# Optimization experiments

Hardware: AMD Instinct MI355X
Metric: run time of the kernel (lower is better)

## Reference

```python
import jax, jax.numpy as jnp
import numpy as np

N = 100000
E = 600000
IN_DIM = 128
HID = 128


def setup_inputs() -> dict:
    key = jax.random.key(0)
    ks = jax.random.split(key, 12)
    def lin(kw, fan_in, fan_out):
        # torch nn.Linear default init: U(-1/sqrt(fan_in), 1/sqrt(fan_in))
        bound = 1.0 / np.sqrt(fan_in)
        kw1, kw2 = jax.random.split(kw)
        w = jax.random.uniform(kw1, (fan_in, fan_out), jnp.float32, -bound, bound)
        b = jax.random.uniform(kw2, (fan_out,), jnp.float32, -bound, bound)
        return w, b
    x = jax.random.normal(ks[0], (N, IN_DIM), jnp.float32)
    edge_index = jax.random.randint(ks[1], (2, E), 0, N, jnp.int64)
    w1a, b1a = lin(ks[2], IN_DIM, HID)
    w1b, b1b = lin(ks[3], HID, HID)
    w2a, b2a = lin(ks[4], HID, HID)
    w2b, b2b = lin(ks[5], HID, HID)
    wo, bo = lin(ks[6], HID, 1)
    return {"x": x, "edge_index": edge_index,
            "w1a": w1a, "b1a": b1a, "w1b": w1b, "b1b": b1b,
            "w2a": w2a, "b2a": b2a, "w2b": w2b, "b2b": b2b,
            "wo": wo, "bo": bo}


def _gin_conv(x, src, dst, wa, ba, wb, bb):
    # sum-aggregate neighbor features: agg[dst] += x[src]; eps = 0 (GIN default)
    agg = jax.ops.segment_sum(x[src], dst, num_segments=N)
    h = x + agg
    h = jax.nn.relu(h @ wa + ba)
    return h @ wb + bb


def reference(x, edge_index, w1a, b1a, w1b, b1b, w2a, b2a, w2b, b2b, wo, bo):
    src, dst = edge_index[0], edge_index[1]
    h = _gin_conv(x, src, dst, w1a, b1a, w1b, b1b)
    h = _gin_conv(h, src, dst, w2a, b2a, w2b, b2b)
    return (h @ wo + bo).squeeze(-1)  # [N]
```

## Files before the change

### kernel.cpp

```cpp
#include <hip/hip_runtime.h>

typedef unsigned short u16;
typedef unsigned int u32;
typedef __bf16 bf16x8 __attribute__((ext_vector_type(8)));
typedef float f32x4 __attribute__((ext_vector_type(4)));

__device__ __forceinline__ u16 f2bf(float f) {
  union { float f; u32 u; } c; c.f = f;
  return (u16)((c.u + 0x7fffu + ((c.u >> 16) & 1u)) >> 16);
}
__device__ __forceinline__ float2 upk2(u32 v) {
  union { u32 u; float f; } a, b; a.u = v << 16; b.u = v & 0xffff0000u;
  return make_float2(a.f, b.f);
}
__device__ __forceinline__ u32 pk2(float x, float y) {
  return (u32)f2bf(x) | ((u32)f2bf(y) << 16);
}

__global__ __launch_bounds__(256) void k_prep(const float4* __restrict__ x4,
                                              uint2* __restrict__ xb,
                                              int n4,
                                              const int* __restrict__ dst,
                                              int* __restrict__ counts,
                                              int E, int histBlocks, int trBlocks,
                                              const float* __restrict__ w0,
                                              const float* __restrict__ w1,
                                              const float* __restrict__ w2,
                                              const float* __restrict__ w3,
                                              u16* __restrict__ wT) {
  int b = blockIdx.x, t = threadIdx.x;
  if ((b % 5) != 4) {
    int cb = b - b / 5;
    int i = cb * 256 + t;
    if (i < n4) {
      float4 v = x4[i];
      xb[i] = make_uint2(pk2(v.x, v.y), pk2(v.z, v.w));
    }
  } else {
    int k = b / 5;
    if (k < histBlocks) {
      int e = k * 256 + t;
      if (e < E) atomicAdd(&counts[dst[e]], 1);
    } else {
      int k2 = k - histBlocks;
      if (k2 < trBlocks) {
        int id = k2 * 256 + t;
        int w = id >> 14, rem = id & 16383;
        int nn = rem >> 7, kk = rem & 127;
        const float* s = (w == 0) ? w0 : (w == 1) ? w1 : (w == 2) ? w2 : w3;
        wT[id] = f2bf(s[kk * 128 + nn]);
      }
    }
  }
}

__global__ __launch_bounds__(256) void k_scan1(const int* __restrict__ counts,
                                               int* __restrict__ excl,
                                               int* __restrict__ partials, int n) {
  __shared__ int sh[256];
  int b = blockIdx.x, t = threadIdx.x;
  int base = b * 1024 + t * 4;
  int v[4];
#pragma unroll
  for (int j = 0; j < 4; ++j) { int i = base + j; v[j] = (i < n) ? counts[i] : 0; }
  int tot = v[0] + v[1] + v[2] + v[3];
  sh[t] = tot; __syncthreads();
  for (int off = 1; off < 256; off <<= 1) {
    int x = (t >= off) ? sh[t - off] : 0;
    __syncthreads();
    sh[t] += x;
    __syncthreads();
  }
  int run = sh[t] - tot;
#pragma unroll
  for (int j = 0; j < 4; ++j) {
    int i = base + j;
    if (i < n) excl[i] = run;
    run += v[j];
  }
  if (t == 255) partials[b] = sh[255];
}

__global__ __launch_bounds__(256) void k_scan23(int* __restrict__ rowstart,
                                                int* __restrict__ cursor,
                                                const int* __restrict__ partials,
                                                int n, int E, int nb) {
  __shared__ int sh[128];
  int t = threadIdx.x;
  int own = 0;
  if (t < 128) { own = (t < nb) ? partials[t] : 0; sh[t] = own; }
  __syncthreads();
  for (int off = 1; off < 128; off <<= 1) {
    int x = (t >= off && t < 128) ? sh[t - off] : 0;
    __syncthreads();
    if (t < 128) sh[t] += x;
    __syncthreads();
  }
  if (t < 128) sh[t] -= own;
  __syncthreads();
  int i = blockIdx.x * 256 + t;
  if (i < n) {
    int v = rowstart[i] + sh[i >> 10];
    rowstart[i] = v;
    cursor[i] = v;
  }
  if (i == 0) rowstart[n] = E;
}

__global__ __launch_bounds__(256) void k_fill(const int* __restrict__ src,
                                              const int* __restrict__ dst,
                                              int* __restrict__ cursor,
                                              int* __restrict__ edge_src, int E) {
  int e = blockIdx.x * 256 + threadIdx.x;
  if (e < E) {
    int d = dst[e];
    int pos = atomicAdd(&cursor[d], 1);
    edge_src[pos] = src[e];
  }
}

__global__ __launch_bounds__(256) void k_agg(const u32* __restrict__ in,
                                             u32* __restrict__ out,
                                             const int* __restrict__ rowstart,
                                             const int* __restrict__ edge_src, int N) {
  int pair = blockIdx.x * 4 + (threadIdx.x >> 6);
  int lane = threadIdx.x & 63;
  int nodeA = __builtin_amdgcn_readfirstlane(pair * 2);
  if (nodeA >= N) return;
  int nodeB = nodeA + 1;
  bool vB = nodeB < N;
  const u32* __restrict__ col = in + lane;
  float2 accA = upk2(col[(size_t)nodeA * 64]);
  float2 accB = vB ? upk2(col[(size_t)nodeB * 64]) : make_float2(0.f, 0.f);
  int a0 = rowstart[nodeA], a1 = rowstart[nodeA + 1];
  int b0 = a1, b1 = vB ? rowstart[nodeB + 1] : a1;
  int ea = a0, eb = b0;
  while (ea < a1 && eb < b1) {
    int ia[8], ib[8]; float wa[8], wb[8]; u32 va[8], vb8[8];
#pragma unroll
    for (int j = 0; j < 8; ++j) {
      int ej = ea + j; int c = (ej < a1) ? ej : (a1 - 1);
      ia[j] = edge_src[c]; wa[j] = (ej < a1) ? 1.f : 0.f;
      int fj = eb + j; int d = (fj < b1) ? fj : (b1 - 1);
      ib[j] = edge_src[d]; wb[j] = (fj < b1) ? 1.f : 0.f;
    }
#pragma unroll
    for (int j = 0; j < 8; ++j) { va[j] = col[(size_t)ia[j] * 64]; vb8[j] = col[(size_t)ib[j] * 64]; }
#pragma unroll
    for (int j = 0; j < 8; ++j) {
      float2 p = upk2(va[j]);
      accA.x = fmaf(wa[j], p.x, accA.x); accA.y = fmaf(wa[j], p.y, accA.y);
      float2 q = upk2(vb8[j]);
      accB.x = fmaf(wb[j], q.x, accB.x); accB.y = fmaf(wb[j], q.y, accB.y);
    }
    ea += 8; eb += 8;
  }
  while (ea < a1) {
    int ia[8]; float wa[8]; u32 va[8];
#pragma unroll
    for (int j = 0; j < 8; ++j) {
      int ej = ea + j; int c = (ej < a1) ? ej : (a1 - 1);
      ia[j] = edge_src[c]; wa[j] = (ej < a1) ? 1.f : 0.f;
    }
#pragma unroll
    for (int j = 0; j < 8; ++j) va[j] = col[(size_t)ia[j] * 64];
#pragma unroll
    for (int j = 0; j < 8; ++j) {
      float2 p = upk2(va[j]);
      accA.x = fmaf(wa[j], p.x, accA.x); accA.y = fmaf(wa[j], p.y, accA.y);
    }
    ea += 8;
  }
  while (eb < b1) {
    int ib[8]; float wb[8]; u32 vb8[8];
#pragma unroll
    for (int j = 0; j < 8; ++j) {
      int fj = eb + j; int d = (fj < b1) ? fj : (b1 - 1);
      ib[j] = edge_src[d]; wb[j] = (fj < b1) ? 1.f : 0.f;
    }
#pragma unroll
    for (int j = 0; j < 8; ++j) vb8[j] = col[(size_t)ib[j] * 64];
#pragma unroll
    for (int j = 0; j < 8; ++j) {
      float2 q = upk2(vb8[j]);
      accB.x = fmaf(wb[j], q.x, accB.x); accB.y = fmaf(wb[j], q.y, accB.y);
    }
    eb += 8;
  }
  out[(size_t)nodeA * 64 + lane] = pk2(accA.x, accA.y);
  if (vB) out[(size_t)nodeB * 64 + lane] = pk2(accB.x, accB.y);
}

template <bool HEAD>
__global__ __launch_bounds__(256) void k_mlp(const u16* __restrict__ in,
                                             const u16* __restrict__ wAT,
                                             const float* __restrict__ bA,
                                             const u16* __restrict__ wBT,
                                             const float* __restrict__ bB,
                                             const float* __restrict__ wo,
                                             const float* __restrict__ bo,
                                             void* __restrict__ outp,
                                             int N, int ntiles) {
  __shared__ u16 lA[64 * 128];
  __shared__ u16 lW[2 * 128 * 128];
  const int tid = threadIdx.x;
  const int wave = tid >> 6, lane = tid & 63;
  const int m16 = lane & 15, quad = lane >> 4;

#pragma unroll
  for (int it = 0; it < 16; ++it) {
    int id = it * 256 + tid;
    int m = id >> 11, rem = id & 2047;
    int row = rem >> 4, c = rem & 15;
    const u16* s = m ? wBT : wAT;
    uint4 v = *(const uint4*)&s[row * 128 + c * 8];
    *(uint4*)&lW[m * 16384 + row * 128 + ((c ^ (row & 15)) << 3)] = v;
  }

  float bAr[8], bBr[8], woR[8];
#pragma unroll
  for (int t = 0; t < 8; ++t) {
    bAr[t] = bA[t * 16 + m16];
    bBr[t] = HEAD ? 0.f : bB[t * 16 + m16];
    woR[t] = HEAD ? wo[t * 16 + m16] : 0.f;
  }
  float bBh[8];
#pragma unroll
  for (int t = 0; t < 8; ++t) bBh[t] = HEAD ? bB[t * 16 + m16] : 0.f;
  float boV = HEAD ? bo[0] : 0.f;

  __syncthreads();

  const int mrow = wave * 16 + m16;

  uint4 pf[4];
  auto gload = [&](int tl) {
#pragma unroll
    for (int it = 0; it < 4; ++it) {
      int gr = tl * 64 + wave * 16 + it * 4 + quad;
      uint4 v = make_uint4(0u, 0u, 0u, 0u);
      if (gr < N) v = *(const uint4*)&in[(size_t)gr * 128 + m16 * 8];
      pf[it] = v;
    }
  };

  int tile = blockIdx.x;
  if (tile < ntiles) gload(tile);
  for (; tile < ntiles; tile += gridDim.x) {
#pragma unroll
    for (int it = 0; it < 4; ++it) {
      int row = wave * 16 + it * 4 + quad;
      *(uint4*)&lA[row * 128 + ((m16 ^ (row & 15)) << 3)] = pf[it];
    }
    bf16x8 aF[4];
#pragma unroll
    for (int ks = 0; ks < 4; ++ks)
      aF[ks] = *(const bf16x8*)&lA[mrow * 128 + (((ks * 4 + quad) ^ m16) << 3)];
    int nxt = tile + gridDim.x;
    if (nxt < ntiles) gload(nxt);

    f32x4 acc[8];
#pragma unroll
    for (int t = 0; t < 8; ++t) acc[t] = (f32x4){0.f, 0.f, 0.f, 0.f};
#pragma unroll
    for (int t = 0; t < 8; ++t) {
      int nrow = t * 16 + m16;
#pragma unroll
      for (int ks = 0; ks < 4; ++ks) {
        bf16x8 bF = *(const bf16x8*)&lW[nrow * 128 + (((ks * 4 + quad) ^ m16) << 3)];
        acc[t] = __builtin_amdgcn_mfma_f32_16x16x32_bf16(aF[ks], bF, acc[t], 0, 0, 0);
      }
    }
#pragma unroll
    for (int t = 0; t < 8; ++t) {
      int n = t * 16 + m16;
#pragma unroll
      for (int r = 0; r < 4; ++r) {
        int rloc = quad * 4 + r;
        int absrow = wave * 16 + rloc;
        float v = acc[t][r] + bAr[t];
        v = v > 0.f ? v : 0.f;
        lA[absrow * 128 + ((((n >> 3) ^ rloc) << 3) | (n & 7))] = f2bf(v);
      }
    }
#pragma unroll
    for (int ks = 0; ks < 4; ++ks)
      aF[ks] = *(const bf16x8*)&lA[mrow * 128 + (((ks * 4 + quad) ^ m16) << 3)];
#pragma unroll
    for (int t = 0; t < 8; ++t) acc[t] = (f32x4){0.f, 0.f, 0.f, 0.f};
#pragma unroll
    for (int t = 0; t < 8; ++t) {
      int nrow = t * 16 + m16;
#pragma unroll
      for (int ks = 0; ks < 4; ++ks) {
        bf16x8 bF = *(const bf16x8*)&lW[16384 + nrow * 128 + (((ks * 4 + quad) ^ m16) << 3)];
        acc[t] = __builtin_amdgcn_mfma_f32_16x16x32_bf16(aF[ks], bF, acc[t], 0, 0, 0);
      }
    }
    if (!HEAD) {
#pragma unroll
      for (int t = 0; t < 8; ++t) {
        int n = t * 16 + m16;
#pragma unroll
        for (int r = 0; r < 4; ++r) {
          int rloc = quad * 4 + r;
          int absrow = wave * 16 + rloc;
          float v = acc[t][r] + bBr[t];
          lA[absrow * 128 + ((((n >> 3) ^ rloc) << 3) | (n & 7))] = f2bf(v);
        }
      }
      u16* out = (u16*)outp;
#pragma unroll
      for (int it = 0; it < 4; ++it) {
        int row = wave * 16 + it * 4 + quad;
        int gr = tile * 64 + row;
        if (gr < N) {
          uint4 v = *(const uint4*)&lA[row * 128 + ((m16 ^ (row & 15)) << 3)];
          *(uint4*)&out[(size_t)gr * 128 + m16 * 8] = v;
        }
      }
    } else {
      float* out = (float*)outp;
      float s[4];
#pragma unroll
      for (int r = 0; r < 4; ++r) {
        float v = 0.f;
#pragma unroll
        for (int t = 0; t < 8; ++t) v += (acc[t][r] + bBh[t]) * woR[t];
        s[r] = v;
      }
#pragma unroll
      for (int r = 0; r < 4; ++r) {
        s[r] += __shfl_xor(s[r], 1, 64);
        s[r] += __shfl_xor(s[r], 2, 64);
        s[r] += __shfl_xor(s[r], 4, 64);
        s[r] += __shfl_xor(s[r], 8, 64);
      }
      if (m16 == 0) {
#pragma unroll
        for (int r = 0; r < 4; ++r) {
          int gr = tile * 64 + wave * 16 + quad * 4 + r;
          if (gr < N) out[gr] = s[r] + boV;
        }
      }
    }
  }
}

extern "C" void kernel_launch(void* const* d_in, const int* in_sizes, int n_in,
                              void* d_out, int out_size, void* d_ws, size_t ws_size,
                              hipStream_t stream) {
  const float* x = (const float*)d_in[0];
  const int* ei = (const int*)d_in[1];
  const int E = in_sizes[1] / 2;
  const int N = in_sizes[0] / 128;
  const int* srcI = ei;
  const int* dstI = ei + E;
  const float* w1a = (const float*)d_in[2];
  const float* b1a = (const float*)d_in[3];
  const float* w1b = (const float*)d_in[4];
  const float* b1b = (const float*)d_in[5];
  const float* w2a = (const float*)d_in[6];
  const float* b2a = (const float*)d_in[7];
  const float* w2b = (const float*)d_in[8];
  const float* b2b = (const float*)d_in[9];
  const float* wo = (const float*)d_in[10];
  const float* bo = (const float*)d_in[11];

  char* ws = (char*)d_ws;
  size_t off = 0;
  auto nx = [&](size_t bytes) {
    size_t o = off;
    off += (bytes + 511) & ~(size_t)511;
    return o;
  };
  int* cursor   = (int*)(ws + nx((size_t)N * 4));
  int* rowstart = (int*)(ws + nx((size_t)(N + 1) * 4));
  int* partials = (int*)(ws + nx(4096));
  int* edge_src = (int*)(ws + nx((size_t)E * 4));
  u16* wT       = (u16*)(ws + nx((size_t)4 * 16384 * 2));
  u16* xb       = (u16*)(ws + nx((size_t)N * 128 * 2));
  u16* bufA     = (u16*)(ws + nx((size_t)N * 128 * 2));
  u16* bufB     = (u16*)(ws + nx((size_t)N * 128 * 2));

  const int nb = (N + 1023) >> 10;
  const int n4 = N * 32;
  const int castBlocks = (n4 + 255) / 256;
  const int histBlocks = (E + 255) / 256;
  const int trBlocks = 256;

  int G = (castBlocks * 5 + 3) / 4 + 4;
  if (G < 5 * (histBlocks + trBlocks)) G = 5 * (histBlocks + trBlocks);

  hipMemsetAsync(cursor, 0, (size_t)N * 4, stream);
  k_prep<<<G, 256, 0, stream>>>((const float4*)x, (uint2*)xb, n4,
                                dstI, cursor, E, histBlocks, trBlocks,
                                w1a, w1b, w2a, w2b, wT);
  k_scan1<<<nb, 256, 0, stream>>>(cursor, rowstart, partials, N);
  k_scan23<<<(N + 255) / 256, 256, 0, stream>>>(rowstart, cursor, partials, N, E, nb);
  k_fill<<<(E + 255) / 256, 256, 0, stream>>>(srcI, dstI, cursor, edge_src, E);

  const int aggBlocks = (N + 7) / 8;
  const int ntiles = (N + 63) / 64;
  const int mlpGrid = 512;

  k_agg<<<aggBlocks, 256, 0, stream>>>((const u32*)xb, (u32*)bufA, rowstart, edge_src, N);
  k_mlp<false><<<mlpGrid, 256, 0, stream>>>(bufA, wT, b1a, wT + 16384, b1b,
                                            nullptr, nullptr, bufB, N, ntiles);
  k_agg<<<aggBlocks, 256, 0, stream>>>((const u32*)bufB, (u32*)xb, rowstart, edge_src, N);
  k_mlp<true><<<mlpGrid, 256, 0, stream>>>(xb, wT + 32768, b2a, wT + 49152, b2b,
                                           wo, bo, d_out, N, ntiles);
}
```

Before: 257.5 us.

## Restructure aggregation: one node per wave, 16-byte loads, four edges in parallel

```diff
diff --git a/kernel.cpp b/kernel.cpp
--- a/kernel.cpp
+++ b/kernel.cpp
@@ -119,76 +119,58 @@
   }
 }
 
-__global__ __launch_bounds__(256) void k_agg(const u32* __restrict__ in,
-                                             u32* __restrict__ out,
+__global__ __launch_bounds__(256) void k_agg(const uint4* __restrict__ in,
+                                             uint4* __restrict__ out,
                                              const int* __restrict__ rowstart,
                                              const int* __restrict__ edge_src, int N) {
-  int pair = blockIdx.x * 4 + (threadIdx.x >> 6);
+  int node = __builtin_amdgcn_readfirstlane(blockIdx.x * 4 + (threadIdx.x >> 6));
+  if (node >= N) return;
   int lane = threadIdx.x & 63;
-  int nodeA = __builtin_amdgcn_readfirstlane(pair * 2);
-  if (nodeA >= N) return;
-  int nodeB = nodeA + 1;
-  bool vB = nodeB < N;
-  const u32* __restrict__ col = in + lane;
-  float2 accA = upk2(col[(size_t)nodeA * 64]);
-  float2 accB = vB ? upk2(col[(size_t)nodeB * 64]) : make_float2(0.f, 0.f);
-  int a0 = rowstart[nodeA], a1 = rowstart[nodeA + 1];
-  int b0 = a1, b1 = vB ? rowstart[nodeB + 1] : a1;
-  int ea = a0, eb = b0;
-  while (ea < a1 && eb < b1) {
-    int ia[8], ib[8]; float wa[8], wb[8]; u32 va[8], vb8[8];
-#pragma unroll
-    for (int j = 0; j < 8; ++j) {
-      int ej = ea + j; int c = (ej < a1) ? ej : (a1 - 1);
-      ia[j] = edge_src[c]; wa[j] = (ej < a1) ? 1.f : 0.f;
-      int fj = eb + j; int d = (fj < b1) ? fj : (b1 - 1);
-      ib[j] = edge_src[d]; wb[j] = (fj < b1) ? 1.f : 0.f;
-    }
-#pragma unroll
-    for (int j = 0; j < 8; ++j) { va[j] = col[(size_t)ia[j] * 64]; vb8[j] = col[(size_t)ib[j] * 64]; }
-#pragma unroll
-    for (int j = 0; j < 8; ++j) {
-      float2 p = upk2(va[j]);
-      accA.x = fmaf(wa[j], p.x, accA.x); accA.y = fmaf(wa[j], p.y, accA.y);
-      float2 q = upk2(vb8[j]);
-      accB.x = fmaf(wb[j], q.x, accB.x); accB.y = fmaf(wb[j], q.y, accB.y);
-    }
-    ea += 8; eb += 8;
-  }
-  while (ea < a1) {
-    int ia[8]; float wa[8]; u32 va[8];
-#pragma unroll
-    for (int j = 0; j < 8; ++j) {
-      int ej = ea + j; int c = (ej < a1) ? ej : (a1 - 1);
-      ia[j] = edge_src[c]; wa[j] = (ej < a1) ? 1.f : 0.f;
-    }
-#pragma unroll
-    for (int j = 0; j < 8; ++j) va[j] = col[(size_t)ia[j] * 64];
-#pragma unroll
-    for (int j = 0; j < 8; ++j) {
-      float2 p = upk2(va[j]);
-      accA.x = fmaf(wa[j], p.x, accA.x); accA.y = fmaf(wa[j], p.y, accA.y);
-    }
-    ea += 8;
-  }
-  while (eb < b1) {
-    int ib[8]; float wb[8]; u32 vb8[8];
-#pragma unroll
-    for (int j = 0; j < 8; ++j) {
-      int fj = eb + j; int d = (fj < b1) ? fj : (b1 - 1);
-      ib[j] = edge_src[d]; wb[j] = (fj < b1) ? 1.f : 0.f;
-    }
-#pragma unroll
-    for (int j = 0; j < 8; ++j) vb8[j] = col[(size_t)ib[j] * 64];
-#pragma unroll
-    for (int j = 0; j < 8; ++j) {
-      float2 q = upk2(vb8[j]);
-      accB.x = fmaf(wb[j], q.x, accB.x); accB.y = fmaf(wb[j], q.y, accB.y);
-    }
-    eb += 8;
-  }
-  out[(size_t)nodeA * 64 + lane] = pk2(accA.x, accA.y);
-  if (vB) out[(size_t)nodeB * 64 + lane] = pk2(accB.x, accB.y);
+  int g = lane >> 4, l = lane & 15;
+
+  float acc[8];
+#pragma unroll
+  for (int i = 0; i < 8; ++i) acc[i] = 0.f;
+
+  auto fma8 = [&](uint4 v, float w) {
+    float2 p;
+    p = upk2(v.x); acc[0] = fmaf(w, p.x, acc[0]); acc[1] = fmaf(w, p.y, acc[1]);
+    p = upk2(v.y); acc[2] = fmaf(w, p.x, acc[2]); acc[3] = fmaf(w, p.y, acc[3]);
+    p = upk2(v.z); acc[4] = fmaf(w, p.x, acc[4]); acc[5] = fmaf(w, p.y, acc[5]);
+    p = upk2(v.w); acc[6] = fmaf(w, p.x, acc[6]); acc[7] = fmaf(w, p.y, acc[7]);
+  };
+
+  int e0 = rowstart[node], e1 = rowstart[node + 1];
+  uint4 sv = in[(size_t)node * 16 + l];
+  fma8(sv, (g == 0) ? 1.f : 0.f);
+
+  for (int e = e0; e < e1; e += 8) {
+    int ea = e + g, eb = e + 4 + g;
+    int ca = (ea < e1) ? ea : (e1 - 1);
+    int cb = (eb < e1) ? eb : (e1 - 1);
+    float wa = (ea < e1) ? 1.f : 0.f;
+    float wb = (eb < e1) ? 1.f : 0.f;
+    int ia = edge_src[ca];
+    int ib = edge_src[cb];
+    uint4 va = in[(size_t)ia * 16 + l];
+    uint4 vb = in[(size_t)ib * 16 + l];
+    fma8(va, wa);
+    fma8(vb, wb);
+  }
+
+#pragma unroll
+  for (int i = 0; i < 8; ++i) {
+    acc[i] += __shfl_xor(acc[i], 16, 64);
+    acc[i] += __shfl_xor(acc[i], 32, 64);
+  }
+  if (g == 0) {
+    uint4 o;
+    o.x = pk2(acc[0], acc[1]);
+    o.y = pk2(acc[2], acc[3]);
+    o.z = pk2(acc[4], acc[5]);
+    o.w = pk2(acc[6], acc[7]);
+    out[(size_t)node * 16 + l] = o;
+  }
 }
 
 template <bool HEAD>
@@ -217,16 +199,14 @@
     *(uint4*)&lW[m * 16384 + row * 128 + ((c ^ (row & 15)) << 3)] = v;
   }
 
-  float bAr[8], bBr[8], woR[8];
+  float bAr[8], bBr[8], woR[8], bBh[8];
 #pragma unroll
   for (int t = 0; t < 8; ++t) {
     bAr[t] = bA[t * 16 + m16];
     bBr[t] = HEAD ? 0.f : bB[t * 16 + m16];
     woR[t] = HEAD ? wo[t * 16 + m16] : 0.f;
-  }
-  float bBh[8];
-#pragma unroll
-  for (int t = 0; t < 8; ++t) bBh[t] = HEAD ? bB[t * 16 + m16] : 0.f;
+    bBh[t] = HEAD ? bB[t * 16 + m16] : 0.f;
+  }
   float boV = HEAD ? bo[0] : 0.f;
 
   __syncthreads();
@@ -400,14 +380,14 @@
   k_scan23<<<(N + 255) / 256, 256, 0, stream>>>(rowstart, cursor, partials, N, E, nb);
   k_fill<<<(E + 255) / 256, 256, 0, stream>>>(srcI, dstI, cursor, edge_src, E);
 
-  const int aggBlocks = (N + 7) / 8;
+  const int aggBlocks = (N + 3) / 4;
   const int ntiles = (N + 63) / 64;
   const int mlpGrid = 512;
 
-  k_agg<<<aggBlocks, 256, 0, stream>>>((const u32*)xb, (u32*)bufA, rowstart, edge_src, N);
+  k_agg<<<aggBlocks, 256, 0, stream>>>((const uint4*)xb, (uint4*)bufA, rowstart, edge_src, N);
   k_mlp<false><<<mlpGrid, 256, 0, stream>>>(bufA, wT, b1a, wT + 16384, b1b,
                                             nullptr, nullptr, bufB, N, ntiles);
-  k_agg<<<aggBlocks, 256, 0, stream>>>((const u32*)bufB, (u32*)xb, rowstart, edge_src, N);
+  k_agg<<<aggBlocks, 256, 0, stream>>>((const uint4*)bufB, (uint4*)xb, rowstart, edge_src, N);
   k_mlp<true><<<mlpGrid, 256, 0, stream>>>(xb, wT + 32768, b2a, wT + 49152, b2b,
                                            wo, bo, d_out, N, ntiles);
 }
```

New measurement: 257.7 us. About the same (+0.1%).
